# Kernel optimization log

Hardware: AMD Instinct MI355X
Metric: run time of the kernel (lower is better)

Reference implementation:

```python
import jax, jax.numpy as jnp
import numpy as np

N_HEADS = 32
WINDOW = 128  # each query t attends keys max(0, t-window) .. t inclusive (window+1 keys)


def _sliding_window_attention(x, Wq, Wk, Wv, Wo, n_heads=N_HEADS, window=WINDOW):
    B, T, D = x.shape
    H, dk = n_heads, D // n_heads
    bs = window            # block size = window -> each query block sees exactly 2 key blocks
    assert T % bs == 0
    nb = T // bs

    def heads(y):  # [B,T,D] -> [B,H,T,dk]
        return y.reshape(B, T, H, dk).transpose(0, 2, 1, 3)

    q = heads(x @ Wq.T)
    k = heads(x @ Wk.T)
    v = heads(x @ Wv.T)

    # Block queries: [B,H,nb,bs,dk]
    qb = q.reshape(B, H, nb, bs, dk)
    # Pad one zero block in front of keys/values, then build per-block 2-block windows.
    zpad = jnp.zeros((B, H, bs, dk), dtype=x.dtype)
    kp = jnp.concatenate([zpad, k], axis=2).reshape(B, H, nb + 1, bs, dk)
    vp = jnp.concatenate([zpad, v], axis=2).reshape(B, H, nb + 1, bs, dk)
    kw = jnp.concatenate([kp[:, :, :-1], kp[:, :, 1:]], axis=3)  # [B,H,nb,2bs,dk]
    vw = jnp.concatenate([vp[:, :, :-1], vp[:, :, 1:]], axis=3)

    scale = 1.0 / np.sqrt(dk).astype(np.float32)
    # scores: [B,H,nb,bs,2bs]
    scores = jnp.einsum('bhnrd,bhncd->bhnrc', qb, kw) * scale

    # Banded causal mask. Query global pos = i*bs + r, key global pos = (i-1)*bs + c.
    i = jnp.arange(nb)[:, None, None]
    r = jnp.arange(bs)[None, :, None]
    c = jnp.arange(2 * bs)[None, None, :]
    dist = (bs + r) - c                       # qpos - keypos
    key_global = i * bs - bs + c
    valid = (dist >= 0) & (dist <= window) & (key_global >= 0)  # [nb,bs,2bs]

    scores = jnp.where(valid[None, None], scores, jnp.finfo(scores.dtype).min)
    probs = jax.nn.softmax(scores, axis=-1)
    out = jnp.einsum('bhnrc,bhncd->bhnrd', probs, vw)           # [B,H,nb,bs,dk]
    out = out.reshape(B, H, T, dk).transpose(0, 2, 1, 3).reshape(B, T, D)
    return out @ Wo.T


def setup_inputs() -> dict:
    key = jax.random.key(0)
    ks = jax.random.split(key, 5)
    B, T, D = 2, 4096, 2048
    w_std = 0.02
    return {
        'x':  jax.random.normal(ks[0], (B, T, D), dtype=jnp.float32),
        'Wq': jax.random.normal(ks[1], (D, D), dtype=jnp.float32) * w_std,
        'Wk': jax.random.normal(ks[2], (D, D), dtype=jnp.float32) * w_std,
        'Wv': jax.random.normal(ks[3], (D, D), dtype=jnp.float32) * w_std,
        'Wo': jax.random.normal(ks[4], (D, D), dtype=jnp.float32) * w_std,
    }


def reference(x, Wq, Wk, Wv, Wo):
    return _sliding_window_attention(x, Wq, Wk, Wv, Wo)
```

## Files before the change

### kernel.cpp

```cpp
#include <hip/hip_runtime.h>
#include <hip/hip_bf16.h>

typedef __attribute__((ext_vector_type(8))) short bf16x8;
typedef __attribute__((ext_vector_type(8))) unsigned short ushort8;
typedef __attribute__((ext_vector_type(4))) float f32x4;
typedef __attribute__((ext_vector_type(2))) unsigned int u32x2;

#define MFMA16(a, b, c) __builtin_amdgcn_mfma_f32_16x16x32_bf16(a, b, c, 0, 0, 0)
#define CFENCE() asm volatile("" ::: "memory")

__device__ __forceinline__ unsigned short f2bf(float x) {
    unsigned u = __builtin_bit_cast(unsigned, x);
    u += 0x7FFFu + ((u >> 16) & 1u);
    return (unsigned short)(u >> 16);
}

__device__ __forceinline__ float fexp2(float x) {
#if __has_builtin(__builtin_amdgcn_exp2f)
    return __builtin_amdgcn_exp2f(x);
#else
    return exp2f(x);
#endif
}

__device__ __forceinline__ void gload16(const void* g, void* l) {
    __builtin_amdgcn_global_load_lds((const __attribute__((address_space(1))) void*)g,
                                     (__attribute__((address_space(3))) void*)l, 16, 0, 0);
}

__device__ __forceinline__ void bar() {
    asm volatile("" ::: "memory");
    __builtin_amdgcn_s_barrier();
    asm volatile("" ::: "memory");
}

#define WAITL() do { asm volatile("s_waitcnt lgkmcnt(0)" ::: "memory"); \
                     __builtin_amdgcn_sched_barrier(0); } while (0)

__global__ void cvt_all(const float* __restrict__ x, const float* __restrict__ wq,
                        const float* __restrict__ wk, const float* __restrict__ wv,
                        const float* __restrict__ wo, unsigned short* __restrict__ dst,
                        int total8) {
    constexpr int XE8 = 2097152;
    constexpr int WE8 = 524288;
    int stride = gridDim.x * blockDim.x;
    for (int i = blockIdx.x * blockDim.x + threadIdx.x; i < total8; i += stride) {
        const float* src;
        if (i < XE8) {
            src = x + (size_t)i * 8;
        } else {
            int k = i - XE8;
            int seg = k >> 19;
            int off = k & (WE8 - 1);
            const float* w = (seg == 0) ? wq : (seg == 1) ? wk : (seg == 2) ? wv : wo;
            src = w + (size_t)off * 8;
        }
        const float4* s = (const float4*)src;
        float4 a = s[0], b = s[1];
        ushort8 o;
        o[0] = f2bf(a.x); o[1] = f2bf(a.y); o[2] = f2bf(a.z); o[3] = f2bf(a.w);
        o[4] = f2bf(b.x); o[5] = f2bf(b.y); o[6] = f2bf(b.z); o[7] = f2bf(b.w);
        *(reinterpret_cast<ushort8*>(dst) + i) = o;
    }
}

#define QUAD(mg, ng, bfv)                                                         \
    do {                                                                          \
        _Pragma("unroll") for (int mm = 0; mm < 4; ++mm)                          \
        _Pragma("unroll") for (int nn = 0; nn < 2; ++nn)                          \
        _Pragma("unroll") for (int kk = 0; kk < 2; ++kk)                          \
            acc[(mg) * 4 + mm][(ng) * 2 + nn] =                                   \
                MFMA16(af[mm][kk], bfv[nn][kk], acc[(mg) * 4 + mm][(ng) * 2 + nn]); \
    } while (0)

template <int MODE>
__global__ __launch_bounds__(512, 2)
void gemm256(const unsigned short* __restrict__ A, const unsigned short* __restrict__ B,
             void* __restrict__ C, int M, int N, int K) {
    __shared__ char sm[131072];

    const int tid  = threadIdx.x;
    const int wid  = tid >> 6, lane = tid & 63;
    const int wr   = wid >> 2, wc = wid & 3;
    const int lrow = lane >> 4, lcol = lane & 15;

    const int nbm = M >> 8;
    const int rpx = nbm >> 3;
    const int xcd = blockIdx.x & 7;
    const int l   = blockIdx.x >> 3;
    const int bm  = xcd * rpx + (l & (rpx - 1));
    const int bn  = l / rpx;

    const int srow = wid * 8 + (lane >> 3);
    const int scol = ((lane & 7) ^ ((lane >> 3) & 7)) * 8;
    const unsigned short* aS = A + (size_t)(bm * 256 + srow) * K + scol;
    const unsigned short* bS = B + (size_t)(bn * 256 + srow) * K + scol;
    const int ldsW = wid * 1024;

    auto stageA = [&](int d, int h, int t) {
#pragma unroll
        for (int q = 0; q < 2; ++q)
            gload16(aS + (size_t)(h * 128 + q * 64) * K + t * 64,
                    sm + d * 32768 + h * 16384 + ldsW + q * 8192);
    };
    auto stageB = [&](int d, int h, int t) {
#pragma unroll
        for (int q = 0; q < 2; ++q)
            gload16(bS + (size_t)(h * 128 + q * 64) * K + t * 64,
                    sm + 65536 + d * 32768 + h * 16384 + ldsW + q * 8192);
    };

    const int swz0 = (lrow * 16) ^ ((lcol & 7) << 4);
    const int swz1 = (64 + lrow * 16) ^ ((lcol & 7) << 4);
    const int ra = wr * 16 + lcol;
    const int rb = wc * 16 + lcol;

    bf16x8 af[4][2], bl[2][2], bh[2][2];
    auto loadA = [&](int d, int mg) {
#pragma unroll
        for (int mm = 0; mm < 4; ++mm) {
            af[mm][0] = *(const bf16x8*)(sm + d * 32768 + mg * 16384 + (mm * 32 + ra) * 128 + swz0);
            af[mm][1] = *(const bf16x8*)(sm + d * 32768 + mg * 16384 + (mm * 32 + ra) * 128 + swz1);
        }
    };
    auto loadB = [&](int d, int ng, bf16x8 (&bfv)[2][2]) {
#pragma unroll
        for (int nn = 0; nn < 2; ++nn) {
            bfv[nn][0] = *(const bf16x8*)(sm + 65536 + d * 32768 + ng * 16384 + (nn * 64 + rb) * 128 + swz0);
            bfv[nn][1] = *(const bf16x8*)(sm + 65536 + d * 32768 + ng * 16384 + (nn * 64 + rb) * 128 + swz1);
        }
    };

    f32x4 acc[8][4] = {};

    stageA(0, 0, 0); stageB(0, 0, 0); stageB(0, 1, 0); stageA(0, 1, 0);
    stageA(1, 0, 1); stageB(1, 0, 1); stageB(1, 1, 1); stageA(1, 1, 1);
    asm volatile("s_waitcnt vmcnt(8)" ::: "memory");
    bar();

    const int NI = K / 128;
#pragma unroll 1
    for (int i = 0; i < NI; ++i) {
        const int t0 = 2 * i;
        const bool last = (i == NI - 1);
        loadA(0, 0); loadB(0, 0, bl);
        bar(); WAITL();
        __builtin_amdgcn_s_setprio(1); QUAD(0, 0, bl); __builtin_amdgcn_s_setprio(0);
        bar();
        loadB(0, 1, bh);
        if (!last) stageA(0, 0, t0 + 2);
        bar(); WAITL();
        __builtin_amdgcn_s_setprio(1); QUAD(0, 1, bh); __builtin_amdgcn_s_setprio(0);
        bar();
        loadA(0, 1);
        if (!last) stageB(0, 0, t0 + 2);
        bar(); WAITL();
        __builtin_amdgcn_s_setprio(1); QUAD(1, 0, bl); __builtin_amdgcn_s_setprio(0);
        bar();
        if (!last) { stageB(0, 1, t0 + 2); stageA(0, 1, t0 + 2); }
        bar();
        __builtin_amdgcn_s_setprio(1); QUAD(1, 1, bh); __builtin_amdgcn_s_setprio(0);
        if (last) asm volatile("s_waitcnt vmcnt(0)" ::: "memory");
        else      asm volatile("s_waitcnt vmcnt(8)" ::: "memory");
        bar();
        loadA(1, 0); loadB(1, 0, bl);
        bar(); WAITL();
        __builtin_amdgcn_s_setprio(1); QUAD(0, 0, bl); __builtin_amdgcn_s_setprio(0);
        bar();
        loadB(1, 1, bh);
        if (!last) stageA(1, 0, t0 + 3);
        bar(); WAITL();
        __builtin_amdgcn_s_setprio(1); QUAD(0, 1, bh); __builtin_amdgcn_s_setprio(0);
        bar();
        loadA(1, 1);
        if (!last) stageB(1, 0, t0 + 3);
        bar(); WAITL();
        __builtin_amdgcn_s_setprio(1); QUAD(1, 0, bl); __builtin_amdgcn_s_setprio(0);
        bar();
        if (!last) { stageB(1, 1, t0 + 3); stageA(1, 1, t0 + 3); }
        bar();
        __builtin_amdgcn_s_setprio(1); QUAD(1, 1, bh); __builtin_amdgcn_s_setprio(0);
        if (!last) asm volatile("s_waitcnt vmcnt(8)" ::: "memory");
        bar();
    }

    const size_t row0 = (size_t)bm * 256 + wr * 16 + lrow * 4;
    if (MODE == 1) {
        const int col0 = bn * 256 + wc * 16 + lcol;
#pragma unroll
        for (int m = 0; m < 8; ++m)
#pragma unroll
            for (int n = 0; n < 4; ++n)
#pragma unroll
                for (int r = 0; r < 4; ++r)
                    ((float*)C)[(row0 + m * 32 + r) * N + col0 + n * 64] = acc[m][n][r];
    } else {
        const int seg = (bn * 256) >> 11;
        const int coll = bn * 256 - seg * 2048 + wc * 16 + lcol;
        unsigned short* out = (unsigned short*)C + (size_t)seg * 16777216ull;
#pragma unroll
        for (int m = 0; m < 8; ++m)
#pragma unroll
            for (int n = 0; n < 4; ++n)
#pragma unroll
                for (int r = 0; r < 4; ++r)
                    out[(row0 + m * 32 + r) * 2048 + coll + n * 64] = f2bf(acc[m][n][r]);
    }
}

__global__ __launch_bounds__(256, 3)
void swa_attn(const unsigned short* __restrict__ Qb, const unsigned short* __restrict__ Kb,
              const unsigned short* __restrict__ Vb, unsigned short* __restrict__ Ob) {
    constexpr int T = 4096, D = 2048;
    constexpr float SC = 0.18033688011112042f;

    __shared__ unsigned short vt[64][136];
    __shared__ unsigned short pls[4][32][40];

    const int bid  = blockIdx.x;
    const int flat = (bid & 7) * 256 + (bid >> 3);
    const int i = flat & 31, h = (flat >> 5) & 31, b = flat >> 10;

    const int tid = threadIdx.x, wid = tid >> 6, lane = tid & 63;
    const int lcol = lane & 15, lrow = lane >> 4;

    const unsigned short* qp = Qb + (size_t)b * T * D + h * 64;
    const unsigned short* kp = Kb + (size_t)b * T * D + h * 64;
    const unsigned short* vp = Vb + (size_t)b * T * D + h * 64;

    const int t0 = (i == 0) ? 1 : 0;

    const int q0 = i * 128 + wid * 32;
    bf16x8 aq[2][2];
#pragma unroll
    for (int qg = 0; qg < 2; ++qg)
#pragma unroll
        for (int kf = 0; kf < 2; ++kf)
            aq[qg][kf] = *(const bf16x8*)(qp + (size_t)(q0 + qg * 16 + lcol) * D + kf * 32 + lrow * 8);

    f32x4 oacc[2][4] = {};
    float mrun[2] = {-1e30f, -1e30f}, lrun[2] = {0.f, 0.f};

#pragma unroll 1
    for (int t = t0; t < 2; ++t) {
        const int kt0 = (i - 1 + t) * 128;

#pragma unroll
        for (int it = 0; it < 4; ++it) {
            int e = it * 2048 + tid * 8;
            int kr = e >> 6;
            int dc = e & 63;
            bf16x8 v = *(const bf16x8*)(vp + (size_t)(kt0 + kr) * D + dc);
#pragma unroll
            for (int j = 0; j < 8; ++j) vt[dc + j][kr] = (unsigned short)v[j];
        }

        f32x4 s[2][8];
#pragma unroll
        for (int n = 0; n < 8; ++n) {
            const unsigned short* krow = kp + (size_t)(kt0 + n * 16 + lcol) * D + lrow * 8;
            bf16x8 k0 = *(const bf16x8*)(krow);
            bf16x8 k1 = *(const bf16x8*)(krow + 32);
            f32x4 z = {0.f, 0.f, 0.f, 0.f};
            s[0][n] = MFMA16(k1, aq[0][1], MFMA16(k0, aq[0][0], z));
            s[1][n] = MFMA16(k1, aq[1][1], MFMA16(k0, aq[1][0], z));
        }

#pragma unroll
        for (int qg = 0; qg < 2; ++qg) {
            const int q = wid * 32 + qg * 16 + lcol;
#pragma unroll
            for (int n = 0; n < 8; ++n) {
                const int cb = t * 128 + n * 16 + lrow * 4 - q;
#pragma unroll
                for (int r = 0; r < 4; ++r)
                    s[qg][n][r] = ((unsigned)(cb + r) <= 128u) ? s[qg][n][r] * SC : -1e30f;
            }
        }

#pragma unroll
        for (int qg = 0; qg < 2; ++qg) {
            float cm = -1e30f;
#pragma unroll
            for (int n = 0; n < 8; ++n)
#pragma unroll
                for (int r = 0; r < 4; ++r) cm = fmaxf(cm, s[qg][n][r]);
            cm = fmaxf(cm, __shfl_xor(cm, 16));
            cm = fmaxf(cm, __shfl_xor(cm, 32));
            const float mn = fmaxf(mrun[qg], cm);
            const float sf = fexp2(mrun[qg] - mn);
            mrun[qg] = mn;
            float rs = 0.f;
#pragma unroll
            for (int n = 0; n < 8; ++n)
#pragma unroll
                for (int r = 0; r < 4; ++r) {
                    float p = fexp2(s[qg][n][r] - mn);
                    s[qg][n][r] = p;
                    rs += p;
                }
            rs += __shfl_xor(rs, 16);
            rs += __shfl_xor(rs, 32);
            lrun[qg] = lrun[qg] * sf + rs;
#pragma unroll
            for (int nf = 0; nf < 4; ++nf) oacc[qg][nf] *= sf;
        }

        __syncthreads();

#pragma unroll
        for (int ks = 0; ks < 4; ++ks) {
            CFENCE();
#pragma unroll
            for (int qg = 0; qg < 2; ++qg) {
                unsigned short* prow = &pls[wid][qg * 16 + lcol][0];
#pragma unroll
                for (int r = 0; r < 4; ++r) {
                    prow[4 * lrow + r]      = f2bf(s[qg][2 * ks][r]);
                    prow[16 + 4 * lrow + r] = f2bf(s[qg][2 * ks + 1][r]);
                }
            }
            CFENCE();
            WAITL();
            bf16x8 pf0 = *(const bf16x8*)&pls[wid][lcol][lrow * 8];
            bf16x8 pf1 = *(const bf16x8*)&pls[wid][16 + lcol][lrow * 8];
#pragma unroll
            for (int nf = 0; nf < 4; ++nf) {
                bf16x8 av = *(const bf16x8*)&vt[nf * 16 + lcol][ks * 32 + lrow * 8];
                oacc[0][nf] = MFMA16(av, pf0, oacc[0][nf]);
                oacc[1][nf] = MFMA16(av, pf1, oacc[1][nf]);
            }
            CFENCE();
        }

        __syncthreads();
    }

#pragma unroll
    for (int qg = 0; qg < 2; ++qg) {
        const float inv = 1.f / lrun[qg];
        const int tok = i * 128 + wid * 32 + qg * 16 + lcol;
        unsigned short* orow = Ob + (size_t)(b * T + tok) * D + h * 64;
#pragma unroll
        for (int nf = 0; nf < 4; ++nf) {
            unsigned o0 = (unsigned)f2bf(oacc[qg][nf][0] * inv) |
                          ((unsigned)f2bf(oacc[qg][nf][1] * inv) << 16);
            unsigned o1 = (unsigned)f2bf(oacc[qg][nf][2] * inv) |
                          ((unsigned)f2bf(oacc[qg][nf][3] * inv) << 16);
            *(u32x2*)(orow + nf * 16 + lrow * 4) = (u32x2){o0, o1};
        }
    }
}

extern "C" void kernel_launch(void* const* d_in, const int* in_sizes, int n_in,
                              void* d_out, int out_size, void* d_ws, size_t ws_size,
                              hipStream_t stream) {
    const float* x  = (const float*)d_in[0];
    const float* Wq = (const float*)d_in[1];
    const float* Wk = (const float*)d_in[2];
    const float* Wv = (const float*)d_in[3];
    const float* Wo = (const float*)d_in[4];

    constexpr int B = 2, T = 4096, D = 2048;
    constexpr int M = B * T;
    constexpr size_t XE = (size_t)M * D;
    constexpr size_t WE = (size_t)D * D;

    char* ws = (char*)d_ws;
    unsigned short* xb  = (unsigned short*)(ws);
    unsigned short* wqb = (unsigned short*)(ws + XE * 2);
    unsigned short* qb  = (unsigned short*)(ws + XE * 2 + WE * 8);
    unsigned short* kb  = (unsigned short*)(ws + XE * 4 + WE * 8);
    unsigned short* vb  = (unsigned short*)(ws + XE * 6 + WE * 8);
    unsigned short* ab  = (unsigned short*)(ws + XE * 8 + WE * 8);

    cvt_all<<<2048, 256, 0, stream>>>(x, Wq, Wk, Wv, Wo, xb, (int)((XE + 4 * WE) / 8));

    gemm256<2><<<dim3((M / 256) * (6144 / 256)), 512, 0, stream>>>(xb, wqb, qb, M, 6144, D);

    swa_attn<<<dim3(2048), 256, 0, stream>>>(qb, kb, vb, ab);

    gemm256<1><<<dim3((M / 256) * (D / 256)), 512, 0, stream>>>(ab, wqb + 3 * WE, d_out, M, D, D);
}
```

Before: 357.3 us.

## Restage GEMM operands through a five-slot LDS ring of half-tiles

```diff
diff --git a/kernel.cpp b/kernel.cpp
--- a/kernel.cpp
+++ b/kernel.cpp
@@ -77,7 +77,7 @@
 __global__ __launch_bounds__(512, 2)
 void gemm256(const unsigned short* __restrict__ A, const unsigned short* __restrict__ B,
              void* __restrict__ C, int M, int N, int K) {
-    __shared__ char sm[131072];
+    __shared__ char sm[163840];
 
     const int tid  = threadIdx.x;
     const int wid  = tid >> 6, lane = tid & 63;
@@ -97,17 +97,17 @@
     const unsigned short* bS = B + (size_t)(bn * 256 + srow) * K + scol;
     const int ldsW = wid * 1024;
 
-    auto stageA = [&](int d, int h, int t) {
+    auto stageAh = [&](int slot, int h, int T) {
 #pragma unroll
         for (int q = 0; q < 2; ++q)
-            gload16(aS + (size_t)(h * 128 + q * 64) * K + t * 64,
-                    sm + d * 32768 + h * 16384 + ldsW + q * 8192);
+            gload16(aS + (size_t)(h * 128 + q * 64) * K + T * 64,
+                    sm + slot * 32768 + ldsW + q * 8192);
     };
-    auto stageB = [&](int d, int h, int t) {
+    auto stageBh = [&](int slot, int h, int T) {
 #pragma unroll
         for (int q = 0; q < 2; ++q)
-            gload16(bS + (size_t)(h * 128 + q * 64) * K + t * 64,
-                    sm + 65536 + d * 32768 + h * 16384 + ldsW + q * 8192);
+            gload16(bS + (size_t)(h * 128 + q * 64) * K + T * 64,
+                    sm + slot * 32768 + 16384 + ldsW + q * 8192);
     };
 
     const int swz0 = (lrow * 16) ^ ((lcol & 7) << 4);
@@ -116,72 +116,58 @@
     const int rb = wc * 16 + lcol;
 
     bf16x8 af[4][2], bl[2][2], bh[2][2];
-    auto loadA = [&](int d, int mg) {
+    auto loadA = [&](int slot) {
+        const char* base = sm + slot * 32768;
 #pragma unroll
         for (int mm = 0; mm < 4; ++mm) {
-            af[mm][0] = *(const bf16x8*)(sm + d * 32768 + mg * 16384 + (mm * 32 + ra) * 128 + swz0);
-            af[mm][1] = *(const bf16x8*)(sm + d * 32768 + mg * 16384 + (mm * 32 + ra) * 128 + swz1);
+            af[mm][0] = *(const bf16x8*)(base + (mm * 32 + ra) * 128 + swz0);
+            af[mm][1] = *(const bf16x8*)(base + (mm * 32 + ra) * 128 + swz1);
         }
     };
-    auto loadB = [&](int d, int ng, bf16x8 (&bfv)[2][2]) {
+    auto loadB = [&](int slot, bf16x8 (&bfv)[2][2]) {
+        const char* base = sm + slot * 32768 + 16384;
 #pragma unroll
         for (int nn = 0; nn < 2; ++nn) {
-            bfv[nn][0] = *(const bf16x8*)(sm + 65536 + d * 32768 + ng * 16384 + (nn * 64 + rb) * 128 + swz0);
-            bfv[nn][1] = *(const bf16x8*)(sm + 65536 + d * 32768 + ng * 16384 + (nn * 64 + rb) * 128 + swz1);
+            bfv[nn][0] = *(const bf16x8*)(base + (nn * 64 + rb) * 128 + swz0);
+            bfv[nn][1] = *(const bf16x8*)(base + (nn * 64 + rb) * 128 + swz1);
         }
     };
 
     f32x4 acc[8][4] = {};
 
-    stageA(0, 0, 0); stageB(0, 0, 0); stageB(0, 1, 0); stageA(0, 1, 0);
-    stageA(1, 0, 1); stageB(1, 0, 1); stageB(1, 1, 1); stageA(1, 1, 1);
+    stageAh(0, 0, 0); stageBh(0, 0, 0);
+    stageAh(1, 1, 0); stageBh(1, 1, 0);
+    stageAh(2, 0, 1); stageBh(2, 0, 1);
+    stageAh(3, 1, 1); stageBh(3, 1, 1);
     asm volatile("s_waitcnt vmcnt(8)" ::: "memory");
     bar();
 
-    const int NI = K / 128;
+    const int NI = K / 64;
+    int s0 = 0, s1 = 1;
 #pragma unroll 1
-    for (int i = 0; i < NI; ++i) {
-        const int t0 = 2 * i;
-        const bool last = (i == NI - 1);
-        loadA(0, 0); loadB(0, 0, bl);
+    for (int t = 0; t < NI; ++t) {
+        const bool st = (t < NI - 2);
+        const int sX = s0 ? s0 - 1 : 4;
+        loadA(s0); loadB(s0, bl);
+        if (st) { stageAh(sX, 0, t + 2); stageBh(sX, 0, t + 2); }
         bar(); WAITL();
         __builtin_amdgcn_s_setprio(1); QUAD(0, 0, bl); __builtin_amdgcn_s_setprio(0);
         bar();
-        loadB(0, 1, bh);
-        if (!last) stageA(0, 0, t0 + 2);
+        loadB(s1, bh);
+        if (st) { stageAh(s0, 1, t + 2); stageBh(s0, 1, t + 2); }
         bar(); WAITL();
         __builtin_amdgcn_s_setprio(1); QUAD(0, 1, bh); __builtin_amdgcn_s_setprio(0);
         bar();
-        loadA(0, 1);
-        if (!last) stageB(0, 0, t0 + 2);
+        loadA(s1);
         bar(); WAITL();
         __builtin_amdgcn_s_setprio(1); QUAD(1, 0, bl); __builtin_amdgcn_s_setprio(0);
         bar();
-        if (!last) { stageB(0, 1, t0 + 2); stageA(0, 1, t0 + 2); }
+        __builtin_amdgcn_s_setprio(1); QUAD(1, 1, bh); __builtin_amdgcn_s_setprio(0);
+        if (t == NI - 2)      asm volatile("s_waitcnt vmcnt(0)" ::: "memory");
+        else if (t < NI - 2)  asm volatile("s_waitcnt vmcnt(8)" ::: "memory");
         bar();
-        __builtin_amdgcn_s_setprio(1); QUAD(1, 1, bh); __builtin_amdgcn_s_setprio(0);
-        if (last) asm volatile("s_waitcnt vmcnt(0)" ::: "memory");
-        else      asm volatile("s_waitcnt vmcnt(8)" ::: "memory");
-        bar();
-        loadA(1, 0); loadB(1, 0, bl);
-        bar(); WAITL();
-        __builtin_amdgcn_s_setprio(1); QUAD(0, 0, bl); __builtin_amdgcn_s_setprio(0);
-        bar();
-        loadB(1, 1, bh);
-        if (!last) stageA(1, 0, t0 + 3);
-        bar(); WAITL();
-        __builtin_amdgcn_s_setprio(1); QUAD(0, 1, bh); __builtin_amdgcn_s_setprio(0);
-        bar();
-        loadA(1, 1);
-        if (!last) stageB(1, 0, t0 + 3);
-        bar(); WAITL();
-        __builtin_amdgcn_s_setprio(1); QUAD(1, 0, bl); __builtin_amdgcn_s_setprio(0);
-        bar();
-        if (!last) { stageB(1, 1, t0 + 3); stageA(1, 1, t0 + 3); }
-        bar();
-        __builtin_amdgcn_s_setprio(1); QUAD(1, 1, bh); __builtin_amdgcn_s_setprio(0);
-        if (!last) asm volatile("s_waitcnt vmcnt(8)" ::: "memory");
-        bar();
+        s0 += 2; if (s0 >= 5) s0 -= 5;
+        s1 += 2; if (s1 >= 5) s1 -= 5;
     }
 
     const size_t row0 = (size_t)bm * 256 + wr * 16 + lrow * 4;
```

Result: no change. 356.1 us (-0.3%).
